# Kernel tuning notes

Hardware: AMD Instinct MI355X
Metric: run time of the kernel (lower is better)

The kernel has to match this reference:

```python
import jax, jax.numpy as jnp
import numpy as np

B, S, H = 2, 2048, 2048
NH, NKV, HD = 16, 4, 128
EPS = 1e-6


def setup_inputs() -> dict:
    key = jax.random.key(0)
    ks = jax.random.split(key, 8)
    s = 0.02
    x = jax.random.normal(ks[0], (B, S, H), dtype=jnp.float32)
    # real rotary tables: cos/sin of shape [S, HD]
    inv_freq = 1.0 / (10000.0 ** (np.arange(0, HD, 2, dtype=np.float32) / HD))
    t = np.arange(S, dtype=np.float32)
    freqs = np.outer(t, inv_freq)              # [S, HD/2]
    emb = np.concatenate([freqs, freqs], axis=-1)  # [S, HD]
    rotary_cos = jnp.asarray(np.cos(emb))
    rotary_sin = jnp.asarray(np.sin(emb))
    Wq = jax.random.normal(ks[1], (H, NH * HD), dtype=jnp.float32) * s
    Wk = jax.random.normal(ks[2], (H, NKV * HD), dtype=jnp.float32) * s
    Wv = jax.random.normal(ks[3], (H, NKV * HD), dtype=jnp.float32) * s
    Wo = jax.random.normal(ks[4], (H, H), dtype=jnp.float32) * s
    q_norm_w = jnp.ones((HD,), dtype=jnp.float32)
    k_norm_w = jnp.ones((HD,), dtype=jnp.float32)
    return {"x": x, "rotary_cos": rotary_cos, "rotary_sin": rotary_sin,
            "Wq": Wq, "Wk": Wk, "Wv": Wv, "Wo": Wo,
            "q_norm_w": q_norm_w, "k_norm_w": k_norm_w}


def _rms_norm(x, w):
    return x * jax.lax.rsqrt(jnp.mean(x * x, axis=-1, keepdims=True) + EPS) * w


def _rotate_half(x):
    half = x.shape[-1] // 2
    return jnp.concatenate([-x[..., half:], x[..., :half]], axis=-1)


def reference(x, rotary_cos, rotary_sin, Wq, Wk, Wv, Wo, q_norm_w, k_norm_w):
    b, s, _ = x.shape
    q = (x @ Wq).reshape(b, s, NH, HD)
    k = (x @ Wk).reshape(b, s, NKV, HD)
    v = (x @ Wv).reshape(b, s, NKV, HD)
    q = _rms_norm(q, q_norm_w)
    k = _rms_norm(k, k_norm_w)
    cos = rotary_cos[None, :, None, :]  # [1,S,1,HD]
    sin = rotary_sin[None, :, None, :]
    q = q * cos + _rotate_half(q) * sin
    k = k * cos + _rotate_half(k) * sin
    # GQA: repeat kv heads
    rep = NH // NKV
    k = jnp.repeat(k, rep, axis=2)  # [b,s,NH,HD]
    v = jnp.repeat(v, rep, axis=2)
    scores = jnp.einsum('bqhd,bkhd->bhqk', q, k) / jnp.sqrt(jnp.float32(HD))
    causal = jnp.tril(jnp.ones((s, s), dtype=bool))
    scores = jnp.where(causal[None, None], scores, -jnp.inf)
    probs = jax.nn.softmax(scores.astype(jnp.float32), axis=-1).astype(q.dtype)
    y = jnp.einsum('bhqk,bkhd->bqhd', probs, v).reshape(b, s, NH * HD)
    return y @ Wo
```

## Files before the change

kernel.cpp:

```cpp
#include <hip/hip_runtime.h>


#define S_LEN 2048

typedef __bf16 bf16_t;
typedef bf16_t bf16x8 __attribute__((ext_vector_type(8)));
typedef float f32x4 __attribute__((ext_vector_type(4)));
typedef float f32x16 __attribute__((ext_vector_type(16)));
typedef unsigned int u32x4 __attribute__((ext_vector_type(4)));
typedef unsigned short u16x4 __attribute__((ext_vector_type(4)));

__device__ __forceinline__ unsigned short f2bf(float f) {
  unsigned int u = __builtin_bit_cast(unsigned int, f);
  u += 0x7fffu + ((u >> 16) & 1u);
  return (unsigned short)(u >> 16);
}
__device__ __forceinline__ float bf2f(unsigned short h) {
  return __builtin_bit_cast(float, (unsigned int)h << 16);
}
__device__ __forceinline__ unsigned pk2(float a, float b) {
  return (unsigned)f2bf(a) | ((unsigned)f2bf(b) << 16);
}
__device__ __forceinline__ unsigned cvtpk(float a, float b) {
  unsigned r;
  asm("v_cvt_pk_bf16_f32 %0, %1, %2" : "=v"(r) : "v"(a), "v"(b));
  return r;
}

typedef const __attribute__((address_space(1))) unsigned int* gas1_t;
typedef __attribute__((address_space(3))) unsigned int* las3_t;
__device__ __forceinline__ void async16(const void* g, void* l) {
  __builtin_amdgcn_global_load_lds((gas1_t)g, (las3_t)l, 16, 0, 0);
}

__device__ __forceinline__ bf16x8 ldfrag(const void* p) {
  return __builtin_bit_cast(bf16x8, *(const u32x4*)p);
}
__device__ __forceinline__ f32x16 mfma32(bf16x8 a, bf16x8 b, f32x16 c) {
  return __builtin_amdgcn_mfma_f32_32x32x16_bf16(a, b, c, 0, 0, 0);
}
__device__ __forceinline__ f32x16 zero16() {
  f32x16 v;
#pragma unroll
  for (int i = 0; i < 16; i++) v[i] = 0.f;
  return v;
}

__device__ __forceinline__ void transpose_body(
    const float* __restrict__ in, unsigned short* __restrict__ out,
    int C, int out_row_off, int out_ld, int bx, int by, int t,
    unsigned short (*L)[68]) {
  int r0 = by * 64, c0 = bx * 64;
#pragma unroll
  for (int i = 0; i < 4; i++) {
    int r = i * 16 + (t >> 4);
    int c = (t & 15) * 4;
    f32x4 v = *(const f32x4*)&in[(size_t)(r0 + r) * C + c0 + c];
    u16x4 u;
    u.x = f2bf(v.x); u.y = f2bf(v.y); u.z = f2bf(v.z); u.w = f2bf(v.w);
    *(u16x4*)&L[r][c] = u;
  }
  __syncthreads();
#pragma unroll
  for (int i = 0; i < 4; i++) {
    int oc = i * 16 + (t >> 4);
    int orr = (t & 15) * 4;
    u16x4 u;
    u.x = L[orr + 0][oc]; u.y = L[orr + 1][oc];
    u.z = L[orr + 2][oc]; u.w = L[orr + 3][oc];
    *(u16x4*)&out[(size_t)(c0 + oc + out_row_off) * out_ld + r0 + orr] = u;
  }
}

__global__ __launch_bounds__(256) void prep_kernel(
    const float* __restrict__ x, const float* __restrict__ Wq,
    const float* __restrict__ Wk, const float* __restrict__ Wv,
    const float* __restrict__ Wo, unsigned short* __restrict__ xb,
    unsigned short* __restrict__ WT, unsigned short* __restrict__ WoT) {
  __shared__ unsigned short L[64][68];
  const int bid = blockIdx.x, t = threadIdx.x;
  if (bid < 4096) {
    int i = bid * 256 + t;
    const f32x4* p = (const f32x4*)x + (size_t)i * 2;
    f32x4 a = p[0], b = p[1];
    u32x4 o;
    o.x = pk2(a.x, a.y);
    o.y = pk2(a.z, a.w);
    o.z = pk2(b.x, b.y);
    o.w = pk2(b.z, b.w);
    *(u32x4*)(xb + (size_t)i * 8) = o;
  } else if (bid < 5120) {
    int id = bid - 4096;
    transpose_body(Wq, WT, 2048, 0, 2048, id & 31, id >> 5, t, L);
  } else if (bid < 5376) {
    int id = bid - 5120;
    transpose_body(Wk, WT, 512, 2048, 2048, id & 7, id >> 3, t, L);
  } else if (bid < 5632) {
    int id = bid - 5376;
    transpose_body(Wv, WT, 512, 2560, 2048, id & 7, id >> 3, t, L);
  } else {
    int id = bid - 5632;
    transpose_body(Wo, WoT, 2048, 0, 2048, id & 31, id >> 5, t, L);
  }
}

__global__ __launch_bounds__(256) void gemm_bf16_kernel(
    const unsigned short* __restrict__ A, const unsigned short* __restrict__ Bt,
    void* __restrict__ Cout, int M, int N, int K, int out_bf16) {
  __shared__ unsigned short As[2][128 * 32];
  __shared__ unsigned short Bs[2][128 * 32];
  const int t = threadIdx.x, w = t >> 6, l = t & 63;
  const int wr = w >> 1, wc = w & 1;
  const int lrow = l & 15, lhi = l >> 4;
  const int row0 = blockIdx.y * 128, col0 = blockIdx.x * 128;
  const unsigned short* Ab = A + (size_t)row0 * K;
  const unsigned short* Bb = Bt + (size_t)col0 * K;
  const int srow = w * 32 + (l >> 2);
  const int scol = (l & 3) * 8;
  f32x4 z = {0.f, 0.f, 0.f, 0.f};
  f32x4 acc[4][4];
#pragma unroll
  for (int m = 0; m < 4; m++)
#pragma unroll
    for (int n = 0; n < 4; n++) acc[m][n] = z;

#define STAGE_G(tt, buf)                                                        \
  {                                                                             \
    const int k0_ = (tt) * 32;                                                  \
    async16(Ab + (size_t)srow * K + k0_ + scol,        &As[buf][(w * 32) * 32]);\
    async16(Ab + (size_t)(srow + 16) * K + k0_ + scol, &As[buf][(w * 32 + 16) * 32]); \
    async16(Bb + (size_t)srow * K + k0_ + scol,        &Bs[buf][(w * 32) * 32]);\
    async16(Bb + (size_t)(srow + 16) * K + k0_ + scol, &Bs[buf][(w * 32 + 16) * 32]); \
  }

  STAGE_G(0, 0);
  const int NT = K >> 5;
  for (int tt = 0; tt < NT; tt++) {
    const int cur = tt & 1;
    if (tt + 1 < NT) {
      STAGE_G(tt + 1, cur ^ 1);
      asm volatile("s_waitcnt vmcnt(4)" ::: "memory");
    } else {
      asm volatile("s_waitcnt vmcnt(0)" ::: "memory");
    }
    __builtin_amdgcn_s_barrier();
    __builtin_amdgcn_sched_barrier(0);
    bf16x8 af[4], bfr[4];
#pragma unroll
    for (int m = 0; m < 4; m++)
      af[m] = ldfrag(&As[cur][(wr * 64 + m * 16 + lrow) * 32 + lhi * 8]);
#pragma unroll
    for (int n = 0; n < 4; n++)
      bfr[n] = ldfrag(&Bs[cur][(wc * 64 + n * 16 + lrow) * 32 + lhi * 8]);
    __builtin_amdgcn_s_setprio(1);
#pragma unroll
    for (int m = 0; m < 4; m++)
#pragma unroll
      for (int n = 0; n < 4; n++)
        acc[m][n] = __builtin_amdgcn_mfma_f32_16x16x32_bf16(af[m], bfr[n], acc[m][n], 0, 0, 0);
    __builtin_amdgcn_s_setprio(0);
    __builtin_amdgcn_sched_barrier(0);
    __builtin_amdgcn_s_barrier();
  }
#undef STAGE_G

  if (out_bf16) {
    unsigned short* C = (unsigned short*)Cout;
#pragma unroll
    for (int m = 0; m < 4; m++)
#pragma unroll
      for (int n = 0; n < 4; n++)
#pragma unroll
        for (int r = 0; r < 4; r++) {
          size_t grow = row0 + wr * 64 + m * 16 + lhi * 4 + r;
          size_t gcol = col0 + wc * 64 + n * 16 + lrow;
          C[grow * N + gcol] = f2bf(acc[m][n][r]);
        }
  } else {
    float* C = (float*)Cout;
#pragma unroll
    for (int m = 0; m < 4; m++)
#pragma unroll
      for (int n = 0; n < 4; n++)
#pragma unroll
        for (int r = 0; r < 4; r++) {
          size_t grow = row0 + wr * 64 + m * 16 + lhi * 4 + r;
          size_t gcol = col0 + wc * 64 + n * 16 + lrow;
          C[grow * N + gcol] = acc[m][n][r];
        }
  }
}

__global__ __launch_bounds__(256) void mid_kernel(
    const unsigned short* __restrict__ QKV, const float* __restrict__ cosT,
    const float* __restrict__ sinT, const float* __restrict__ qw,
    const float* __restrict__ kw, unsigned short* __restrict__ Qpk,
    unsigned short* __restrict__ Kpk, unsigned short* __restrict__ Vpk) {
  int w = threadIdx.x >> 6, l = threadIdx.x & 63;
  int g = blockIdx.x * 4 + w;
  int bs = g / 24, idx = g - bs * 24;
  int b = bs >> 11, s = bs & 2047;
  int d0 = 2 * l;
  unsigned int uu = *(const unsigned int*)(QKV + (size_t)bs * 3072 + idx * 128 + d0);
  float x0 = bf2f((unsigned short)(uu & 0xffffu));
  float x1 = bf2f((unsigned short)(uu >> 16));
  if (idx < 20) {
    const float* nw = (idx < 16) ? qw : kw;
    float ss = x0 * x0 + x1 * x1;
#pragma unroll
    for (int mk = 1; mk < 64; mk <<= 1) ss += __shfl_xor(ss, mk);
    float inv = rsqrtf(ss * (1.0f / 128.0f) + 1e-6f);
    float n0 = x0 * inv * nw[d0], n1 = x1 * inv * nw[d0 + 1];
    float p0 = __shfl_xor(n0, 32), p1 = __shfl_xor(n1, 32);
    float sg = (l < 32) ? -1.0f : 1.0f;
    float c0 = cosT[s * 128 + d0], c1 = cosT[s * 128 + d0 + 1];
    float sn0 = sinT[s * 128 + d0], sn1 = sinT[s * 128 + d0 + 1];
    float o0 = n0 * c0 + sg * p0 * sn0;
    float o1 = n1 * c1 + sg * p1 * sn1;
    int mf = d0 >> 4, hi = (d0 >> 3) & 1, j = d0 & 7;
    int blk = s >> 5, r31 = s & 31;
    int foff = (mf * 2 + hi) * 256 + r31 * 8 + j;
    unsigned short* dst;
    if (idx < 16) {
      const float qs = 0.08838834764831845f * 1.4426950408889634f;
      o0 *= qs; o1 *= qs;
      dst = Qpk + (((size_t)(b * 16 + idx)) * 64 + blk) * 4096 + foff;
    } else {
      dst = Kpk + (((size_t)(b * 4 + (idx - 16))) * 64 + blk) * 4096 + foff;
    }
    *(unsigned int*)dst = pk2(o0, o1);
  } else {
    int kvh = idx - 20;
    int blk = s >> 5, ks = (s >> 4) & 1, his = (s >> 3) & 1, j = s & 7;
    int n = d0 >> 5, d31 = d0 & 31;
    size_t base = (((size_t)(b * 4 + kvh)) * 64 + blk) * 4096 +
                  (((n * 2 + ks) * 2 + his) * 256 + d31 * 8 + j);
    Vpk[base] = f2bf(x0);
    Vpk[base + 8] = f2bf(x1);
  }
}

__global__ __launch_bounds__(512) void attn_kernel(
    const unsigned short* __restrict__ Qpk, const unsigned short* __restrict__ Kpk,
    const unsigned short* __restrict__ Vpk, unsigned short* __restrict__ Y) {
  __shared__ __attribute__((aligned(16))) unsigned char lds_raw[100352];
  const int t = threadIdx.x, w = t >> 6, l = t & 63;
  const int q31 = l & 31, hi = l >> 5;
  const int grp = w >> 2, hw = w & 3;
  const int bid = blockIdx.x;
  const int xcd = bid & 7;
  const int b = xcd >> 2, kvh = xcd & 3;
  const int hd = kvh * 4 + hw;
  const int bh = b * 16 + hd;
  const int pj = bid >> 3;
  const unsigned short* Kg = Kpk + (size_t)(b * 4 + kvh) * 262144;
  const unsigned short* Vg = Vpk + (size_t)(b * 4 + kvh) * 262144;
  float* mlb = (float*)(lds_raw + 98304);

#define STAGE1(st, buf)                                                        \
  {                                                                            \
    unsigned char* base_ = lds_raw + ((buf) * 2 + grp) * 16384;                \
    const unsigned short* kg_ = Kg + (size_t)(st) * 4096;                      \
    const unsigned short* vg_ = Vg + (size_t)(st) * 4096;                      \
    _Pragma("unroll")                                                          \
    for (int i_ = 0; i_ < 4; i_++) {                                           \
      int c_ = hw * 4 + i_;                                                    \
      const unsigned short* src_ = (c_ < 8) ? (kg_ + c_ * 512 + l * 8)         \
                                            : (vg_ + (c_ - 8) * 512 + l * 8);  \
      async16(src_, base_ + c_ * 1024 + l * 16);                               \
    }                                                                          \
  }

  for (int phase = 0; phase < 2; phase++) {
    const int strip = phase ? pj : (63 - pj);
    const int q0w = strip * 32;
    const int qg = q0w + q31;
    const int nt = strip + 1;
    const int hcut = (nt + 1) >> 1;
    const int myFirst = grp ? hcut : 0;
    const int myCnt = grp ? (nt - hcut) : hcut;
    const int R = hcut;

    const unsigned short* Qs = Qpk + (((size_t)bh * 64 + strip) * 4096) + (size_t)l * 8;
    bf16x8 qf[8];
#pragma unroll
    for (int mf = 0; mf < 8; mf++) qf[mf] = ldfrag(Qs + mf * 512);
    asm volatile("s_waitcnt vmcnt(0)" ::: "memory");

    { int st0 = (myCnt > 0) ? myFirst : 0; STAGE1(st0, 0); }

    f32x16 o[4];
#pragma unroll
    for (int n = 0; n < 4; n++) o[n] = zero16();
    float m = -3.0e38f, lsum = 0.f;

    for (int r = 0; r < R; r++) {
      const int buf = r % 3;
      { int st = (r + 1 < myCnt) ? (myFirst + r + 1) : 0; STAGE1(st, (r + 1) % 3); }
      asm volatile("s_waitcnt vmcnt(4)" ::: "memory");
      __builtin_amdgcn_s_barrier();
      __builtin_amdgcn_sched_barrier(0);

      if (r < myCnt) {
        const int ti = myFirst + r;
        const int kv0 = ti << 5;
        const unsigned short* base =
            (const unsigned short*)(lds_raw + (buf * 2 + grp) * 16384);
        f32x16 sA = zero16(), sB = zero16();
        __builtin_amdgcn_s_setprio(1);
#pragma unroll
        for (int mf = 0; mf < 4; mf++) {
          sA = mfma32(ldfrag(base + mf * 512 + l * 8), qf[mf], sA);
          sB = mfma32(ldfrag(base + (mf + 4) * 512 + l * 8), qf[mf + 4], sB);
        }
        __builtin_amdgcn_s_setprio(0);
#pragma unroll
        for (int rr = 0; rr < 16; rr++) sA[rr] += sB[rr];
        if (ti == nt - 1) {
#pragma unroll
          for (int rr = 0; rr < 16; rr++) {
            int kv = kv0 + (rr & 3) + 8 * (rr >> 2) + 4 * hi;
            if (kv > qg) sA[rr] = -3.0e38f;
          }
        }
        float a0 = fmaxf(sA[0], sA[1]),   a1 = fmaxf(sA[2], sA[3]);
        float a2 = fmaxf(sA[4], sA[5]),   a3 = fmaxf(sA[6], sA[7]);
        float a4 = fmaxf(sA[8], sA[9]),   a5 = fmaxf(sA[10], sA[11]);
        float a6 = fmaxf(sA[12], sA[13]), a7 = fmaxf(sA[14], sA[15]);
        a0 = fmaxf(fmaxf(a0, a1), a2);
        a3 = fmaxf(fmaxf(a3, a4), a5);
        a6 = fmaxf(a6, a7);
        float pm = fmaxf(fmaxf(a0, a3), a6);
        pm = fmaxf(pm, __shfl_xor(pm, 32));
        if (__any(pm > m + 8.0f)) {
          float mn = fmaxf(m, pm);
          float scl = exp2f(m - mn);
          m = mn; lsum *= scl;
#pragma unroll
          for (int rr = 0; rr < 16; rr++) {
            float sr = __shfl(scl, (rr & 3) + 8 * (rr >> 2) + 4 * hi);
            o[0][rr] *= sr; o[1][rr] *= sr; o[2][rr] *= sr; o[3][rr] *= sr;
          }
        }
#pragma unroll
        for (int rr = 0; rr < 16; rr++) sA[rr] = exp2f(sA[rr] - m);
        float s0 = (sA[0] + sA[1]) + (sA[2] + sA[3]);
        float s1 = (sA[4] + sA[5]) + (sA[6] + sA[7]);
        float s2 = (sA[8] + sA[9]) + (sA[10] + sA[11]);
        float s3 = (sA[12] + sA[13]) + (sA[14] + sA[15]);
        float ts = (s0 + s1) + (s2 + s3);
        ts += __shfl_xor(ts, 32);
        lsum += ts;
        bf16x8 paf[2];
#pragma unroll
        for (int f = 0; f < 2; f++) {
          const int bs8 = 8 * f;
          unsigned g00 = cvtpk(sA[bs8 + 0], sA[bs8 + 1]);
          unsigned g01 = cvtpk(sA[bs8 + 2], sA[bs8 + 3]);
          unsigned g10 = cvtpk(sA[bs8 + 4], sA[bs8 + 5]);
          unsigned g11 = cvtpk(sA[bs8 + 6], sA[bs8 + 7]);
          unsigned snd0 = hi ? g00 : g10;
          unsigned snd1 = hi ? g01 : g11;
          unsigned r0 = (unsigned)__shfl_xor((int)snd0, 32);
          unsigned r1 = (unsigned)__shfl_xor((int)snd1, 32);
          unsigned own0 = hi ? g10 : g00;
          unsigned own1 = hi ? g11 : g01;
          u32x4 wv;
          wv.x = hi ? r0 : own0;
          wv.y = hi ? r1 : own1;
          wv.z = hi ? own0 : r0;
          wv.w = hi ? own1 : r1;
          paf[f] = __builtin_bit_cast(bf16x8, wv);
        }
        __builtin_amdgcn_s_setprio(1);
#pragma unroll
        for (int n = 0; n < 4; n++) {
          o[n] = mfma32(paf[0], ldfrag(base + 4096 + (n * 2 + 0) * 512 + l * 8), o[n]);
          o[n] = mfma32(paf[1], ldfrag(base + 4096 + (n * 2 + 1) * 512 + l * 8), o[n]);
        }
        __builtin_amdgcn_s_setprio(0);
      }
    }

    __syncthreads();
    if (l < 32) {
      mlb[hw * 128 + grp * 64 + q31] = m;
      mlb[hw * 128 + grp * 64 + 32 + q31] = lsum;
    }
    __syncthreads();
    float m_o = mlb[hw * 128 + (grp ^ 1) * 64 + q31];
    float l_o = mlb[hw * 128 + (grp ^ 1) * 64 + 32 + q31];
    float M = fmaxf(m, m_o);
    float sc = exp2f(m - M);
    float lF = lsum * sc + l_o * exp2f(m_o - M);
#pragma unroll
    for (int rr = 0; rr < 16; rr++) {
      float sr = __shfl(sc, (rr & 3) + 8 * (rr >> 2) + 4 * hi);
      o[0][rr] *= sr; o[1][rr] *= sr; o[2][rr] *= sr; o[3][rr] *= sr;
    }
    float* ob = (float*)lds_raw + hw * 4096;
    if (grp == 1) {
#pragma unroll
      for (int rr = 0; rr < 16; rr++) {
        int cr = (rr & 3) + 8 * (rr >> 2) + 4 * hi;
#pragma unroll
        for (int n = 0; n < 4; n++) ob[cr * 128 + n * 32 + q31] = o[n][rr];
      }
    }
    __syncthreads();
    if (grp == 0) {
      float linv = 1.0f / lF;
#pragma unroll
      for (int rr = 0; rr < 16; rr++) {
        int cr = (rr & 3) + 8 * (rr >> 2) + 4 * hi;
        float lr = __shfl(linv, cr);
        int qrow = q0w + cr;
        size_t rowoff = ((size_t)(b * S_LEN + qrow)) * 2048 + hd * 128 + q31;
        Y[rowoff]      = f2bf((o[0][rr] + ob[cr * 128 + q31]) * lr);
        Y[rowoff + 32] = f2bf((o[1][rr] + ob[cr * 128 + 32 + q31]) * lr);
        Y[rowoff + 64] = f2bf((o[2][rr] + ob[cr * 128 + 64 + q31]) * lr);
        Y[rowoff + 96] = f2bf((o[3][rr] + ob[cr * 128 + 96 + q31]) * lr);
      }
    }
    __syncthreads();
  }
#undef STAGE1
}

extern "C" void kernel_launch(void* const* d_in, const int* in_sizes, int n_in,
                              void* d_out, int out_size, void* d_ws, size_t ws_size,
                              hipStream_t stream) {
  const float* x  = (const float*)d_in[0];
  const float* rc = (const float*)d_in[1];
  const float* rs = (const float*)d_in[2];
  const float* Wq = (const float*)d_in[3];
  const float* Wk = (const float*)d_in[4];
  const float* Wv = (const float*)d_in[5];
  const float* Wo = (const float*)d_in[6];
  const float* qw = (const float*)d_in[7];
  const float* kw = (const float*)d_in[8];
  float* out = (float*)d_out;
  char* ws = (char*)d_ws;

  unsigned short* xb   = (unsigned short*)(ws + 0);
  unsigned short* WT   = (unsigned short*)(ws + 16777216);
  unsigned short* WoT  = (unsigned short*)(ws + 29360128);
  unsigned short* QKVb = (unsigned short*)(ws + 37748736);
  unsigned short* Qpk  = (unsigned short*)(ws + 0);
  unsigned short* Kpk  = (unsigned short*)(ws + 16777216);
  unsigned short* Vpk  = (unsigned short*)(ws + 20971520);
  unsigned short* Yb   = (unsigned short*)(ws + 37748736);

  prep_kernel<<<6656, 256, 0, stream>>>(x, Wq, Wk, Wv, Wo, xb, WT, WoT);
  gemm_bf16_kernel<<<dim3(24, 32), 256, 0, stream>>>(xb, WT, QKVb, 4096, 3072, 2048, 1);
  mid_kernel<<<24576, 256, 0, stream>>>(QKVb, rc, rs, qw, kw, Qpk, Kpk, Vpk);
  attn_kernel<<<256, 512, 0, stream>>>(Qpk, Kpk, Vpk, Yb);
  gemm_bf16_kernel<<<dim3(16, 32), 256, 0, stream>>>(Yb, WoT, out, 4096, 2048, 2048, 0);
}
```

Before: 220.2 us.

## Process two adjacent query strips per attention block with 1024 threads sharing KV tiles

The attention block grows from 512 to 1024 threads so each block handles a 64-row query pair (two 32-row strips) per phase instead of one strip. Both strips share the same staged K/V tiles in LDS, which halves per-block global loads per query row, and each wave issues half as many async copies. The KV split between the two wave groups is reorganized per strip pair, and the final merge is serialized over the two strips through LDS. The cost is more registers and barriers per block, a lower per-thread register budget at 1024 threads, and some idle iterations for the shorter strip.

```diff
diff --git a/kernel.cpp b/kernel.cpp
--- a/kernel.cpp
+++ b/kernel.cpp
@@ -240,13 +240,14 @@
   }
 }
 
-__global__ __launch_bounds__(512) void attn_kernel(
+__global__ __launch_bounds__(1024) void attn_kernel(
     const unsigned short* __restrict__ Qpk, const unsigned short* __restrict__ Kpk,
     const unsigned short* __restrict__ Vpk, unsigned short* __restrict__ Y) {
-  __shared__ __attribute__((aligned(16))) unsigned char lds_raw[100352];
+  __shared__ __attribute__((aligned(16))) unsigned char lds_raw[102400];
   const int t = threadIdx.x, w = t >> 6, l = t & 63;
   const int q31 = l & 31, hi = l >> 5;
-  const int grp = w >> 2, hw = w & 3;
+  const int hw = w & 3, qh = (w >> 2) & 1, grp = w >> 3;
+  const int unit = hw * 2 + qh;
   const int bid = blockIdx.x;
   const int xcd = bid & 7;
   const int b = xcd >> 2, kvh = xcd & 3;
@@ -263,8 +264,8 @@
     const unsigned short* kg_ = Kg + (size_t)(st) * 4096;                      \
     const unsigned short* vg_ = Vg + (size_t)(st) * 4096;                      \
     _Pragma("unroll")                                                          \
-    for (int i_ = 0; i_ < 4; i_++) {                                           \
-      int c_ = hw * 4 + i_;                                                    \
+    for (int i_ = 0; i_ < 2; i_++) {                                           \
+      int c_ = unit * 2 + i_;                                                  \
       const unsigned short* src_ = (c_ < 8) ? (kg_ + c_ * 512 + l * 8)         \
                                             : (vg_ + (c_ - 8) * 512 + l * 8);  \
       async16(src_, base_ + c_ * 1024 + l * 16);                               \
@@ -272,22 +273,22 @@
   }
 
   for (int phase = 0; phase < 2; phase++) {
-    const int strip = phase ? pj : (63 - pj);
-    const int q0w = strip * 32;
+    const int s = phase ? pj : (31 - pj);
+    const int q0w = s * 64 + qh * 32;
     const int qg = q0w + q31;
-    const int nt = strip + 1;
-    const int hcut = (nt + 1) >> 1;
-    const int myFirst = grp ? hcut : 0;
-    const int myCnt = grp ? (nt - hcut) : hcut;
-    const int R = hcut;
-
-    const unsigned short* Qs = Qpk + (((size_t)bh * 64 + strip) * 4096) + (size_t)l * 8;
+    const int myFirst = grp ? (s + 1) : 0;
+    const int myCnt = grp ? (s + qh) : (s + 1);
+    const int lastTi = 2 * s + qh;
+    const int R = s + 1;
+
+    const unsigned short* Qs =
+        Qpk + (((size_t)bh * 64 + (s * 2 + qh)) * 4096) + (size_t)l * 8;
     bf16x8 qf[8];
 #pragma unroll
     for (int mf = 0; mf < 8; mf++) qf[mf] = ldfrag(Qs + mf * 512);
     asm volatile("s_waitcnt vmcnt(0)" ::: "memory");
 
-    { int st0 = (myCnt > 0) ? myFirst : 0; STAGE1(st0, 0); }
+    STAGE1(myFirst, 0);
 
     f32x16 o[4];
 #pragma unroll
@@ -296,8 +297,8 @@
 
     for (int r = 0; r < R; r++) {
       const int buf = r % 3;
-      { int st = (r + 1 < myCnt) ? (myFirst + r + 1) : 0; STAGE1(st, (r + 1) % 3); }
-      asm volatile("s_waitcnt vmcnt(4)" ::: "memory");
+      { int st = (r + 1 < R) ? (myFirst + r + 1) : myFirst; STAGE1(st, (r + 1) % 3); }
+      asm volatile("s_waitcnt vmcnt(2)" ::: "memory");
       __builtin_amdgcn_s_barrier();
       __builtin_amdgcn_sched_barrier(0);
 
@@ -316,7 +317,7 @@
         __builtin_amdgcn_s_setprio(0);
 #pragma unroll
         for (int rr = 0; rr < 16; rr++) sA[rr] += sB[rr];
-        if (ti == nt - 1) {
+        if (ti == lastTi) {
 #pragma unroll
           for (int rr = 0; rr < 16; rr++) {
             int kv = kv0 + (rr & 3) + 8 * (rr >> 2) + 4 * hi;
@@ -384,12 +385,12 @@
 
     __syncthreads();
     if (l < 32) {
-      mlb[hw * 128 + grp * 64 + q31] = m;
-      mlb[hw * 128 + grp * 64 + 32 + q31] = lsum;
+      mlb[(unit * 2 + grp) * 64 + q31] = m;
+      mlb[(unit * 2 + grp) * 64 + 32 + q31] = lsum;
     }
     __syncthreads();
-    float m_o = mlb[hw * 128 + (grp ^ 1) * 64 + q31];
-    float l_o = mlb[hw * 128 + (grp ^ 1) * 64 + 32 + q31];
+    float m_o = mlb[(unit * 2 + (grp ^ 1)) * 64 + q31];
+    float l_o = mlb[(unit * 2 + (grp ^ 1)) * 64 + 32 + q31];
     float M = fmaxf(m, m_o);
     float sc = exp2f(m - M);
     float lF = lsum * sc + l_o * exp2f(m_o - M);
@@ -398,31 +399,34 @@
       float sr = __shfl(sc, (rr & 3) + 8 * (rr >> 2) + 4 * hi);
       o[0][rr] *= sr; o[1][rr] *= sr; o[2][rr] *= sr; o[3][rr] *= sr;
     }
-    float* ob = (float*)lds_raw + hw * 4096;
-    if (grp == 1) {
-#pragma unroll
-      for (int rr = 0; rr < 16; rr++) {
-        int cr = (rr & 3) + 8 * (rr >> 2) + 4 * hi;
-#pragma unroll
-        for (int n = 0; n < 4; n++) ob[cr * 128 + n * 32 + q31] = o[n][rr];
+#pragma unroll
+    for (int step = 0; step < 2; step++) {
+      float* ob = (float*)(lds_raw + hw * 16384);
+      if (qh == step && grp == 1) {
+#pragma unroll
+        for (int rr = 0; rr < 16; rr++) {
+          int cr = (rr & 3) + 8 * (rr >> 2) + 4 * hi;
+#pragma unroll
+          for (int n = 0; n < 4; n++) ob[cr * 128 + n * 32 + q31] = o[n][rr];
+        }
       }
-    }
-    __syncthreads();
-    if (grp == 0) {
-      float linv = 1.0f / lF;
-#pragma unroll
-      for (int rr = 0; rr < 16; rr++) {
-        int cr = (rr & 3) + 8 * (rr >> 2) + 4 * hi;
-        float lr = __shfl(linv, cr);
-        int qrow = q0w + cr;
-        size_t rowoff = ((size_t)(b * S_LEN + qrow)) * 2048 + hd * 128 + q31;
-        Y[rowoff]      = f2bf((o[0][rr] + ob[cr * 128 + q31]) * lr);
-        Y[rowoff + 32] = f2bf((o[1][rr] + ob[cr * 128 + 32 + q31]) * lr);
-        Y[rowoff + 64] = f2bf((o[2][rr] + ob[cr * 128 + 64 + q31]) * lr);
-        Y[rowoff + 96] = f2bf((o[3][rr] + ob[cr * 128 + 96 + q31]) * lr);
+      __syncthreads();
+      if (qh == step && grp == 0) {
+        float linv = 1.0f / lF;
+#pragma unroll
+        for (int rr = 0; rr < 16; rr++) {
+          int cr = (rr & 3) + 8 * (rr >> 2) + 4 * hi;
+          float lr = __shfl(linv, cr);
+          int qrow = q0w + cr;
+          size_t rowoff = ((size_t)(b * S_LEN + qrow)) * 2048 + hd * 128 + q31;
+          Y[rowoff]      = f2bf((o[0][rr] + ob[cr * 128 + q31]) * lr);
+          Y[rowoff + 32] = f2bf((o[1][rr] + ob[cr * 128 + 32 + q31]) * lr);
+          Y[rowoff + 64] = f2bf((o[2][rr] + ob[cr * 128 + 64 + q31]) * lr);
+          Y[rowoff + 96] = f2bf((o[3][rr] + ob[cr * 128 + 96 + q31]) * lr);
+        }
       }
-    }
-    __syncthreads();
+      __syncthreads();
+    }
   }
 #undef STAGE1
 }
@@ -454,6 +458,6 @@
   prep_kernel<<<6656, 256, 0, stream>>>(x, Wq, Wk, Wv, Wo, xb, WT, WoT);
   gemm_bf16_kernel<<<dim3(24, 32), 256, 0, stream>>>(xb, WT, QKVb, 4096, 3072, 2048, 1);
   mid_kernel<<<24576, 256, 0, stream>>>(QKVb, rc, rs, qw, kw, Qpk, Kpk, Vpk);
-  attn_kernel<<<256, 512, 0, stream>>>(Qpk, Kpk, Vpk, Yb);
+  attn_kernel<<<256, 1024, 0, stream>>>(Qpk, Kpk, Vpk, Yb);
   gemm_bf16_kernel<<<dim3(16, 32), 256, 0, stream>>>(Yb, WoT, out, 4096, 2048, 2048, 0);
 }
```

Result: slower. 635.2 us (+188.5%).

## Fuse RMSNorm, RoPE and QKV packing into the QKV GEMM epilogue

Applied to the files above, without the earlier changes.

The QKV projection GEMM now stages its output tile in shared memory and applies the per-head RMS norm, rotary embedding, Q scaling and packed Q/K/V layout writes directly in its epilogue. The separate mid kernel and the bf16 QKV intermediate buffer are removed. This is meant to save a kernel launch and a full write and read of the intermediate through global memory. In exchange the GEMM epilogue becomes longer and serialized per row, and it uses more shared memory, which could lower occupancy.

```diff
diff --git a/kernel.cpp b/kernel.cpp
--- a/kernel.cpp
+++ b/kernel.cpp
@@ -106,9 +106,14 @@
 
 __global__ __launch_bounds__(256) void gemm_bf16_kernel(
     const unsigned short* __restrict__ A, const unsigned short* __restrict__ Bt,
-    void* __restrict__ Cout, int M, int N, int K, int out_bf16) {
-  __shared__ unsigned short As[2][128 * 32];
-  __shared__ unsigned short Bs[2][128 * 32];
+    void* __restrict__ Cout, int M, int N, int K, int out_bf16,
+    const float* __restrict__ cosT, const float* __restrict__ sinT,
+    const float* __restrict__ qw, const float* __restrict__ kw,
+    unsigned short* __restrict__ Qpk, unsigned short* __restrict__ Kpk,
+    unsigned short* __restrict__ Vpk) {
+  __shared__ __attribute__((aligned(16))) unsigned short shbuf[17408];
+  unsigned short* As = shbuf;
+  unsigned short* Bs = shbuf + 8192;
   const int t = threadIdx.x, w = t >> 6, l = t & 63;
   const int wr = w >> 1, wc = w & 1;
   const int lrow = l & 15, lhi = l >> 4;
@@ -127,10 +132,10 @@
 #define STAGE_G(tt, buf)                                                        \
   {                                                                             \
     const int k0_ = (tt) * 32;                                                  \
-    async16(Ab + (size_t)srow * K + k0_ + scol,        &As[buf][(w * 32) * 32]);\
-    async16(Ab + (size_t)(srow + 16) * K + k0_ + scol, &As[buf][(w * 32 + 16) * 32]); \
-    async16(Bb + (size_t)srow * K + k0_ + scol,        &Bs[buf][(w * 32) * 32]);\
-    async16(Bb + (size_t)(srow + 16) * K + k0_ + scol, &Bs[buf][(w * 32 + 16) * 32]); \
+    async16(Ab + (size_t)srow * K + k0_ + scol,        &As[(buf) * 4096 + (w * 32) * 32]); \
+    async16(Ab + (size_t)(srow + 16) * K + k0_ + scol, &As[(buf) * 4096 + (w * 32 + 16) * 32]); \
+    async16(Bb + (size_t)srow * K + k0_ + scol,        &Bs[(buf) * 4096 + (w * 32) * 32]); \
+    async16(Bb + (size_t)(srow + 16) * K + k0_ + scol, &Bs[(buf) * 4096 + (w * 32 + 16) * 32]); \
   }
 
   STAGE_G(0, 0);
@@ -148,10 +153,10 @@
     bf16x8 af[4], bfr[4];
 #pragma unroll
     for (int m = 0; m < 4; m++)
-      af[m] = ldfrag(&As[cur][(wr * 64 + m * 16 + lrow) * 32 + lhi * 8]);
+      af[m] = ldfrag(&As[cur * 4096 + (wr * 64 + m * 16 + lrow) * 32 + lhi * 8]);
 #pragma unroll
     for (int n = 0; n < 4; n++)
-      bfr[n] = ldfrag(&Bs[cur][(wc * 64 + n * 16 + lrow) * 32 + lhi * 8]);
+      bfr[n] = ldfrag(&Bs[cur * 4096 + (wc * 64 + n * 16 + lrow) * 32 + lhi * 8]);
     __builtin_amdgcn_s_setprio(1);
 #pragma unroll
     for (int m = 0; m < 4; m++)
@@ -164,7 +169,61 @@
   }
 #undef STAGE_G
 
-  if (out_bf16) {
+  if (Qpk) {
+#pragma unroll
+    for (int m = 0; m < 4; m++)
+#pragma unroll
+      for (int n = 0; n < 4; n++)
+#pragma unroll
+        for (int r = 0; r < 4; r++)
+          shbuf[(wr * 64 + m * 16 + lhi * 4 + r) * 136 + wc * 64 + n * 16 + lrow] =
+              f2bf(acc[m][n][r]);
+    __syncthreads();
+    const int head = blockIdx.x;
+    const int d0 = 2 * l;
+    for (int rr = 0; rr < 32; rr++) {
+      const int row = w * 32 + rr;
+      const int bs = row0 + row;
+      const int b = bs >> 11, s = bs & 2047;
+      unsigned int uu = *(const unsigned int*)&shbuf[row * 136 + d0];
+      float x0 = bf2f((unsigned short)(uu & 0xffffu));
+      float x1 = bf2f((unsigned short)(uu >> 16));
+      if (head < 20) {
+        const float* nw = (head < 16) ? qw : kw;
+        float ss = x0 * x0 + x1 * x1;
+#pragma unroll
+        for (int mk = 1; mk < 64; mk <<= 1) ss += __shfl_xor(ss, mk);
+        float inv = rsqrtf(ss * (1.0f / 128.0f) + 1e-6f);
+        float n0 = x0 * inv * nw[d0], n1 = x1 * inv * nw[d0 + 1];
+        float p0 = __shfl_xor(n0, 32), p1 = __shfl_xor(n1, 32);
+        float sg = (l < 32) ? -1.0f : 1.0f;
+        float c0 = cosT[s * 128 + d0], c1 = cosT[s * 128 + d0 + 1];
+        float sn0 = sinT[s * 128 + d0], sn1 = sinT[s * 128 + d0 + 1];
+        float o0 = n0 * c0 + sg * p0 * sn0;
+        float o1 = n1 * c1 + sg * p1 * sn1;
+        int mf = d0 >> 4, hi = (d0 >> 3) & 1, j = d0 & 7;
+        int blk = s >> 5, r31 = s & 31;
+        int foff = (mf * 2 + hi) * 256 + r31 * 8 + j;
+        unsigned short* dst;
+        if (head < 16) {
+          const float qs = 0.08838834764831845f * 1.4426950408889634f;
+          o0 *= qs; o1 *= qs;
+          dst = Qpk + (((size_t)(b * 16 + head)) * 64 + blk) * 4096 + foff;
+        } else {
+          dst = Kpk + (((size_t)(b * 4 + (head - 16))) * 64 + blk) * 4096 + foff;
+        }
+        *(unsigned int*)dst = pk2(o0, o1);
+      } else {
+        int kvh = head - 20;
+        int blk = s >> 5, ks = (s >> 4) & 1, his = (s >> 3) & 1, j = s & 7;
+        int n = d0 >> 5, d31 = d0 & 31;
+        size_t base = (((size_t)(b * 4 + kvh)) * 64 + blk) * 4096 +
+                      (((n * 2 + ks) * 2 + his) * 256 + d31 * 8 + j);
+        Vpk[base] = f2bf(x0);
+        Vpk[base + 8] = f2bf(x1);
+      }
+    }
+  } else if (out_bf16) {
     unsigned short* C = (unsigned short*)Cout;
 #pragma unroll
     for (int m = 0; m < 4; m++)
@@ -188,55 +247,6 @@
           size_t gcol = col0 + wc * 64 + n * 16 + lrow;
           C[grow * N + gcol] = acc[m][n][r];
         }
-  }
-}
-
-__global__ __launch_bounds__(256) void mid_kernel(
-    const unsigned short* __restrict__ QKV, const float* __restrict__ cosT,
-    const float* __restrict__ sinT, const float* __restrict__ qw,
-    const float* __restrict__ kw, unsigned short* __restrict__ Qpk,
-    unsigned short* __restrict__ Kpk, unsigned short* __restrict__ Vpk) {
-  int w = threadIdx.x >> 6, l = threadIdx.x & 63;
-  int g = blockIdx.x * 4 + w;
-  int bs = g / 24, idx = g - bs * 24;
-  int b = bs >> 11, s = bs & 2047;
-  int d0 = 2 * l;
-  unsigned int uu = *(const unsigned int*)(QKV + (size_t)bs * 3072 + idx * 128 + d0);
-  float x0 = bf2f((unsigned short)(uu & 0xffffu));
-  float x1 = bf2f((unsigned short)(uu >> 16));
-  if (idx < 20) {
-    const float* nw = (idx < 16) ? qw : kw;
-    float ss = x0 * x0 + x1 * x1;
-#pragma unroll
-    for (int mk = 1; mk < 64; mk <<= 1) ss += __shfl_xor(ss, mk);
-    float inv = rsqrtf(ss * (1.0f / 128.0f) + 1e-6f);
-    float n0 = x0 * inv * nw[d0], n1 = x1 * inv * nw[d0 + 1];
-    float p0 = __shfl_xor(n0, 32), p1 = __shfl_xor(n1, 32);
-    float sg = (l < 32) ? -1.0f : 1.0f;
-    float c0 = cosT[s * 128 + d0], c1 = cosT[s * 128 + d0 + 1];
-    float sn0 = sinT[s * 128 + d0], sn1 = sinT[s * 128 + d0 + 1];
-    float o0 = n0 * c0 + sg * p0 * sn0;
-    float o1 = n1 * c1 + sg * p1 * sn1;
-    int mf = d0 >> 4, hi = (d0 >> 3) & 1, j = d0 & 7;
-    int blk = s >> 5, r31 = s & 31;
-    int foff = (mf * 2 + hi) * 256 + r31 * 8 + j;
-    unsigned short* dst;
-    if (idx < 16) {
-      const float qs = 0.08838834764831845f * 1.4426950408889634f;
-      o0 *= qs; o1 *= qs;
-      dst = Qpk + (((size_t)(b * 16 + idx)) * 64 + blk) * 4096 + foff;
-    } else {
-      dst = Kpk + (((size_t)(b * 4 + (idx - 16))) * 64 + blk) * 4096 + foff;
-    }
-    *(unsigned int*)dst = pk2(o0, o1);
-  } else {
-    int kvh = idx - 20;
-    int blk = s >> 5, ks = (s >> 4) & 1, his = (s >> 3) & 1, j = s & 7;
-    int n = d0 >> 5, d31 = d0 & 31;
-    size_t base = (((size_t)(b * 4 + kvh)) * 64 + blk) * 4096 +
-                  (((n * 2 + ks) * 2 + his) * 256 + d31 * 8 + j);
-    Vpk[base] = f2bf(x0);
-    Vpk[base + 8] = f2bf(x1);
   }
 }
 
@@ -445,15 +455,16 @@
   unsigned short* xb   = (unsigned short*)(ws + 0);
   unsigned short* WT   = (unsigned short*)(ws + 16777216);
   unsigned short* WoT  = (unsigned short*)(ws + 29360128);
-  unsigned short* QKVb = (unsigned short*)(ws + 37748736);
-  unsigned short* Qpk  = (unsigned short*)(ws + 0);
-  unsigned short* Kpk  = (unsigned short*)(ws + 16777216);
-  unsigned short* Vpk  = (unsigned short*)(ws + 20971520);
-  unsigned short* Yb   = (unsigned short*)(ws + 37748736);
+  unsigned short* Qpk  = (unsigned short*)(ws + 37748736);
+  unsigned short* Kpk  = (unsigned short*)(ws + 54525952);
+  unsigned short* Vpk  = (unsigned short*)(ws + 58720256);
+  unsigned short* Yb   = (unsigned short*)(ws + 0);
 
   prep_kernel<<<6656, 256, 0, stream>>>(x, Wq, Wk, Wv, Wo, xb, WT, WoT);
-  gemm_bf16_kernel<<<dim3(24, 32), 256, 0, stream>>>(xb, WT, QKVb, 4096, 3072, 2048, 1);
-  mid_kernel<<<24576, 256, 0, stream>>>(QKVb, rc, rs, qw, kw, Qpk, Kpk, Vpk);
+  gemm_bf16_kernel<<<dim3(24, 32), 256, 0, stream>>>(
+      xb, WT, nullptr, 4096, 3072, 2048, 1, rc, rs, qw, kw, Qpk, Kpk, Vpk);
   attn_kernel<<<256, 512, 0, stream>>>(Qpk, Kpk, Vpk, Yb);
-  gemm_bf16_kernel<<<dim3(16, 32), 256, 0, stream>>>(Yb, WoT, out, 4096, 2048, 2048, 0);
-}
+  gemm_bf16_kernel<<<dim3(16, 32), 256, 0, stream>>>(
+      Yb, WoT, out, 4096, 2048, 2048, 0, nullptr, nullptr, nullptr, nullptr,
+      nullptr, nullptr, nullptr);
+}
```

After: 211.6 us. 1.04x faster.
